# Kernel optimization log

Hardware: AMD Instinct MI355X
Metric: run time of the kernel (lower is better)

## Reference

```python
import jax, jax.numpy as jnp
import numpy as np

K = 1.0        # Lorentz manifold curvature parameter
EPS = 1e-7     # arccosh argument clamp (geoopt float32 eps)


def projx(x):
    # Project onto the hyperboloid: x0 = sqrt(K + ||x_1:||^2)
    rest = x[..., 1:]
    x0 = jnp.sqrt(K + jnp.sum(rest * rest, axis=-1, keepdims=True))
    return jnp.concatenate([x0, rest], axis=-1)


def setup_inputs() -> dict:
    key = jax.random.key(0)
    k1, k2 = jax.random.split(key)
    B, C, D = 16384, 2048, 512
    x = jax.random.normal(k1, (B, D), dtype=jnp.float32)
    # ManifoldParameter: random_normal with std = 1/sqrt(n_dim)
    points = jax.random.normal(k2, (C, D), dtype=jnp.float32) * (1.0 / np.sqrt(D))
    return {"x": x, "points": points}


def reference(x, points):
    xp = projx(x)        # (B, D) on hyperboloid
    pp = projx(points)   # (C, D) on hyperboloid
    # Minkowski inner <x,p>_L = -x0*p0 + sum_{i>0} x_i p_i = x.p - 2*x0*p0
    # Computed as a GEMM plus a rank-1 correction (avoids (B,C,D) intermediate).
    inner = xp @ pp.T - 2.0 * jnp.outer(xp[:, 0], pp[:, 0])  # (B, C)
    d = jnp.sqrt(K) * jnp.arccosh(jnp.maximum(-inner / K, 1.0 + EPS))
    return -d  # (B, C) negative Riemannian distances (class logits)
```

## Files before the change

kernel.cpp:

```cpp
#include <hip/hip_runtime.h>
#include <hip/hip_bf16.h>
#include <stdint.h>

#define B_ROWS 16384
#define C_ROWS 2048
#define D_FULL 512
#define KP     512

#define BM 128
#define BN 128
#define BK 64

typedef __attribute__((ext_vector_type(8))) short bf16x8;
typedef __attribute__((ext_vector_type(4))) float f32x4;

typedef __attribute__((address_space(1))) void glb_void;
typedef __attribute__((address_space(3))) void lds_void;

__device__ __forceinline__ void gld16(const void* g, void* l) {
    __builtin_amdgcn_global_load_lds((glb_void*)(uintptr_t)g,
                                     (lds_void*)(uintptr_t)l, 16, 0, 0);
}

__global__ __launch_bounds__(256) void prep_kernel(
    const float* __restrict__ x, const float* __restrict__ pts,
    unsigned short* __restrict__ Abf, unsigned short* __restrict__ Bbf,
    float* __restrict__ xn, float* __restrict__ pn)
{
    int row = blockIdx.x;
    const float* src;
    unsigned short* dst;
    float* nrm;
    if (row < B_ROWS) {
        src = x + (size_t)row * D_FULL;
        dst = Abf + (size_t)row * KP;
        nrm = xn + row;
    } else {
        int r = row - B_ROWS;
        src = pts + (size_t)r * D_FULL;
        dst = Bbf + (size_t)r * KP;
        nrm = pn + r;
    }
    int t = threadIdx.x;
    float v0 = src[t + 1];
    float v1 = (t < 255) ? src[t + 257] : 0.0f;
    __hip_bfloat16 b0 = __float2bfloat16(v0);
    __hip_bfloat16 b1 = __float2bfloat16(v1);
    dst[t]       = *(unsigned short*)&b0;
    dst[t + 256] = *(unsigned short*)&b1;
    float ss = v0 * v0 + v1 * v1;
    #pragma unroll
    for (int off = 32; off > 0; off >>= 1) ss += __shfl_down(ss, off);
    __shared__ float red[4];
    if ((t & 63) == 0) red[t >> 6] = ss;
    __syncthreads();
    if (t == 0) nrm[0] = sqrtf(1.0f + red[0] + red[1] + red[2] + red[3]);
}

__global__ __launch_bounds__(256) void gemm_kernel(
    const unsigned short* __restrict__ A,
    const unsigned short* __restrict__ Bm,
    const float* __restrict__ xn, const float* __restrict__ pn,
    float* __restrict__ out)
{
    __shared__ unsigned short As[BM * BK];
    __shared__ unsigned short Bs[BN * BK];

    const int tid  = threadIdx.x;
    const int wave = tid >> 6;
    const int lane = tid & 63;
    const int wm   = wave >> 1;
    const int wn   = wave & 1;
    const int lrow = lane & 15;
    const int quad = lane >> 4;

    const int bm0 = blockIdx.x * BM;
    const int bn0 = blockIdx.y * BN;

    const int srow = wave * 32 + (lane >> 3);
    const int scol = (lane & 7) * 8;

    const unsigned short* gA = A  + (size_t)(bm0 + srow) * KP + scol;
    const unsigned short* gB = Bm + (size_t)(bn0 + srow) * KP + scol;

    f32x4 acc[4][4] = {};

    for (int k0 = 0; k0 < KP; k0 += BK) {
        __syncthreads();
        #pragma unroll
        for (int i = 0; i < 4; ++i) {
            gld16(gA + (size_t)(i * 8) * KP + k0, &As[(wave * 32 + i * 8) * BK]);
            gld16(gB + (size_t)(i * 8) * KP + k0, &Bs[(wave * 32 + i * 8) * BK]);
        }
        __syncthreads();

        #pragma unroll
        for (int kk = 0; kk < BK; kk += 32) {
            bf16x8 af[4], bfr[4];
            #pragma unroll
            for (int mi = 0; mi < 4; ++mi)
                af[mi] = *(const bf16x8*)&As[(wm * 64 + mi * 16 + lrow) * BK + kk + quad * 8];
            #pragma unroll
            for (int ni = 0; ni < 4; ++ni)
                bfr[ni] = *(const bf16x8*)&Bs[(wn * 64 + ni * 16 + lrow) * BK + kk + quad * 8];
            #pragma unroll
            for (int mi = 0; mi < 4; ++mi)
                #pragma unroll
                for (int ni = 0; ni < 4; ++ni)
                    acc[mi][ni] = __builtin_amdgcn_mfma_f32_16x16x32_bf16(
                        af[mi], bfr[ni], acc[mi][ni], 0, 0, 0);
        }
    }

    float pv[4];
    #pragma unroll
    for (int ni = 0; ni < 4; ++ni)
        pv[ni] = pn[bn0 + wn * 64 + ni * 16 + lrow];

    #pragma unroll
    for (int mi = 0; mi < 4; ++mi) {
        #pragma unroll
        for (int r = 0; r < 4; ++r) {
            int row = bm0 + wm * 64 + mi * 16 + quad * 4 + r;
            float xv = xn[row];
            size_t base = (size_t)row * C_ROWS + bn0 + wn * 64 + lrow;
            #pragma unroll
            for (int ni = 0; ni < 4; ++ni) {
                float z = fmaf(xv, pv[ni], -acc[mi][ni][r]);
                z = fmaxf(z, 1.0f + 1e-7f);
                out[base + ni * 16] = -__logf(z + __fsqrt_rn(z * z - 1.0f));
            }
        }
    }
}

extern "C" void kernel_launch(void* const* d_in, const int* in_sizes, int n_in,
                              void* d_out, int out_size, void* d_ws, size_t ws_size,
                              hipStream_t stream) {
    const float* x   = (const float*)d_in[0];
    const float* pts = (const float*)d_in[1];
    float* out = (float*)d_out;

    char* ws = (char*)d_ws;
    unsigned short* Abf = (unsigned short*)ws;
    unsigned short* Bbf = (unsigned short*)(ws + (size_t)B_ROWS * KP * 2);
    float* xn = (float*)(ws + (size_t)(B_ROWS + C_ROWS) * KP * 2);
    float* pn = (float*)((char*)xn + (size_t)B_ROWS * 4);
    (void)in_sizes; (void)n_in; (void)out_size; (void)ws_size;

    prep_kernel<<<B_ROWS + C_ROWS, 256, 0, stream>>>(x, pts, Abf, Bbf, xn, pn);

    dim3 grid(B_ROWS / BM, C_ROWS / BN);
    gemm_kernel<<<grid, 256, 0, stream>>>(Abf, Bbf, xn, pn, out);
}
```

Baseline: 209.0 us.

## Load GEMM fragments directly from global memory with register prefetch

```diff
diff --git a/kernel.cpp b/kernel.cpp
--- a/kernel.cpp
+++ b/kernel.cpp
@@ -9,18 +9,9 @@
 
 #define BM 128
 #define BN 128
-#define BK 64
 
 typedef __attribute__((ext_vector_type(8))) short bf16x8;
 typedef __attribute__((ext_vector_type(4))) float f32x4;
-
-typedef __attribute__((address_space(1))) void glb_void;
-typedef __attribute__((address_space(3))) void lds_void;
-
-__device__ __forceinline__ void gld16(const void* g, void* l) {
-    __builtin_amdgcn_global_load_lds((glb_void*)(uintptr_t)g,
-                                     (lds_void*)(uintptr_t)l, 16, 0, 0);
-}
 
 __global__ __launch_bounds__(256) void prep_kernel(
     const float* __restrict__ x, const float* __restrict__ pts,
@@ -42,12 +33,14 @@
         nrm = pn + r;
     }
     int t = threadIdx.x;
-    float v0 = src[t + 1];
-    float v1 = (t < 255) ? src[t + 257] : 0.0f;
+    float v0 = src[2 * t + 1];
+    float v1 = (t < 255) ? src[2 * t + 2] : 0.0f;
     __hip_bfloat16 b0 = __float2bfloat16(v0);
     __hip_bfloat16 b1 = __float2bfloat16(v1);
-    dst[t]       = *(unsigned short*)&b0;
-    dst[t + 256] = *(unsigned short*)&b1;
+    union { unsigned short u[2]; unsigned int w; } pack;
+    pack.u[0] = *(unsigned short*)&b0;
+    pack.u[1] = *(unsigned short*)&b1;
+    *(unsigned int*)&dst[2 * t] = pack.w;
     float ss = v0 * v0 + v1 * v1;
     #pragma unroll
     for (int off = 32; off > 0; off >>= 1) ss += __shfl_down(ss, off);
@@ -63,9 +56,6 @@
     const float* __restrict__ xn, const float* __restrict__ pn,
     float* __restrict__ out)
 {
-    __shared__ unsigned short As[BM * BK];
-    __shared__ unsigned short Bs[BN * BK];
-
     const int tid  = threadIdx.x;
     const int wave = tid >> 6;
     const int lane = tid & 63;
@@ -74,43 +64,49 @@
     const int lrow = lane & 15;
     const int quad = lane >> 4;
 
-    const int bm0 = blockIdx.x * BM;
-    const int bn0 = blockIdx.y * BN;
+    const int bn0 = blockIdx.x * BN;
+    const int bm0 = blockIdx.y * BM;
 
-    const int srow = wave * 32 + (lane >> 3);
-    const int scol = (lane & 7) * 8;
-
-    const unsigned short* gA = A  + (size_t)(bm0 + srow) * KP + scol;
-    const unsigned short* gB = Bm + (size_t)(bn0 + srow) * KP + scol;
+    const unsigned short* aBase[4];
+    const unsigned short* bBase[4];
+    #pragma unroll
+    for (int i = 0; i < 4; ++i) {
+        aBase[i] = A  + (size_t)(bm0 + wm * 64 + i * 16 + lrow) * KP + quad * 8;
+        bBase[i] = Bm + (size_t)(bn0 + wn * 64 + i * 16 + lrow) * KP + quad * 8;
+    }
 
     f32x4 acc[4][4] = {};
 
-    for (int k0 = 0; k0 < KP; k0 += BK) {
-        __syncthreads();
+    bf16x8 a_cur[4], b_cur[4];
+    #pragma unroll
+    for (int i = 0; i < 4; ++i) {
+        a_cur[i] = *(const bf16x8*)(aBase[i]);
+        b_cur[i] = *(const bf16x8*)(bBase[i]);
+    }
+
+    #pragma unroll 2
+    for (int k = 32; k < KP; k += 32) {
+        bf16x8 a_nxt[4], b_nxt[4];
         #pragma unroll
         for (int i = 0; i < 4; ++i) {
-            gld16(gA + (size_t)(i * 8) * KP + k0, &As[(wave * 32 + i * 8) * BK]);
-            gld16(gB + (size_t)(i * 8) * KP + k0, &Bs[(wave * 32 + i * 8) * BK]);
+            a_nxt[i] = *(const bf16x8*)(aBase[i] + k);
+            b_nxt[i] = *(const bf16x8*)(bBase[i] + k);
         }
-        __syncthreads();
-
         #pragma unroll
-        for (int kk = 0; kk < BK; kk += 32) {
-            bf16x8 af[4], bfr[4];
-            #pragma unroll
-            for (int mi = 0; mi < 4; ++mi)
-                af[mi] = *(const bf16x8*)&As[(wm * 64 + mi * 16 + lrow) * BK + kk + quad * 8];
+        for (int mi = 0; mi < 4; ++mi)
             #pragma unroll
             for (int ni = 0; ni < 4; ++ni)
-                bfr[ni] = *(const bf16x8*)&Bs[(wn * 64 + ni * 16 + lrow) * BK + kk + quad * 8];
-            #pragma unroll
-            for (int mi = 0; mi < 4; ++mi)
-                #pragma unroll
-                for (int ni = 0; ni < 4; ++ni)
-                    acc[mi][ni] = __builtin_amdgcn_mfma_f32_16x16x32_bf16(
-                        af[mi], bfr[ni], acc[mi][ni], 0, 0, 0);
-        }
+                acc[mi][ni] = __builtin_amdgcn_mfma_f32_16x16x32_bf16(
+                    a_cur[mi], b_cur[ni], acc[mi][ni], 0, 0, 0);
+        #pragma unroll
+        for (int i = 0; i < 4; ++i) { a_cur[i] = a_nxt[i]; b_cur[i] = b_nxt[i]; }
     }
+    #pragma unroll
+    for (int mi = 0; mi < 4; ++mi)
+        #pragma unroll
+        for (int ni = 0; ni < 4; ++ni)
+            acc[mi][ni] = __builtin_amdgcn_mfma_f32_16x16x32_bf16(
+                a_cur[mi], b_cur[ni], acc[mi][ni], 0, 0, 0);
 
     float pv[4];
     #pragma unroll
@@ -150,6 +146,6 @@
 
     prep_kernel<<<B_ROWS + C_ROWS, 256, 0, stream>>>(x, pts, Abf, Bbf, xn, pn);
 
-    dim3 grid(B_ROWS / BM, C_ROWS / BN);
+    dim3 grid(C_ROWS / BN, B_ROWS / BM);
     gemm_kernel<<<grid, 256, 0, stream>>>(Abf, Bbf, xn, pn, out);
 }
```

Measured after the change: 277.1 us. +32.6%, slower.

## Double-buffer LDS tiles with swizzled layout and vectorize prep stores

Applied to the files above, without the earlier changes.

```diff
diff --git a/kernel.cpp b/kernel.cpp
--- a/kernel.cpp
+++ b/kernel.cpp
@@ -9,7 +9,7 @@
 
 #define BM 128
 #define BN 128
-#define BK 64
+#define BK 32
 
 typedef __attribute__((ext_vector_type(8))) short bf16x8;
 typedef __attribute__((ext_vector_type(4))) float f32x4;
@@ -42,12 +42,14 @@
         nrm = pn + r;
     }
     int t = threadIdx.x;
-    float v0 = src[t + 1];
-    float v1 = (t < 255) ? src[t + 257] : 0.0f;
+    float v0 = src[2 * t + 1];
+    float v1 = (t < 255) ? src[2 * t + 2] : 0.0f;
     __hip_bfloat16 b0 = __float2bfloat16(v0);
     __hip_bfloat16 b1 = __float2bfloat16(v1);
-    dst[t]       = *(unsigned short*)&b0;
-    dst[t + 256] = *(unsigned short*)&b1;
+    union { unsigned short u[2]; unsigned int w; } pack;
+    pack.u[0] = *(unsigned short*)&b0;
+    pack.u[1] = *(unsigned short*)&b1;
+    *(unsigned int*)&dst[2 * t] = pack.w;
     float ss = v0 * v0 + v1 * v1;
     #pragma unroll
     for (int off = 32; off > 0; off >>= 1) ss += __shfl_down(ss, off);
@@ -63,8 +65,8 @@
     const float* __restrict__ xn, const float* __restrict__ pn,
     float* __restrict__ out)
 {
-    __shared__ unsigned short As[BM * BK];
-    __shared__ unsigned short Bs[BN * BK];
+    __shared__ unsigned short As[2][BM * BK];
+    __shared__ unsigned short Bs[2][BN * BK];
 
     const int tid  = threadIdx.x;
     const int wave = tid >> 6;
@@ -77,39 +79,57 @@
     const int bm0 = blockIdx.x * BM;
     const int bn0 = blockIdx.y * BN;
 
-    const int srow = wave * 32 + (lane >> 3);
-    const int scol = (lane & 7) * 8;
+    const int srow  = lane >> 2;
+    const int schk  = (lane & 3) ^ (srow & 3) ^ ((lane >> 4) & 3);
+    const int scol  = schk << 3;
 
-    const unsigned short* gA = A  + (size_t)(bm0 + srow) * KP + scol;
-    const unsigned short* gB = Bm + (size_t)(bn0 + srow) * KP + scol;
+    const unsigned short* gA0 = A  + (size_t)(bm0 + wave * 32 + srow) * KP + scol;
+    const unsigned short* gA1 = gA0 + (size_t)16 * KP;
+    const unsigned short* gB0 = Bm + (size_t)(bn0 + wave * 32 + srow) * KP + scol;
+    const unsigned short* gB1 = gB0 + (size_t)16 * KP;
+
+    unsigned short* ldsA0 = &As[0][(wave * 32 + 0) * BK];
+    unsigned short* ldsA1 = &As[0][(wave * 32 + 16) * BK];
+    unsigned short* ldsB0 = &Bs[0][(wave * 32 + 0) * BK];
+    unsigned short* ldsB1 = &Bs[0][(wave * 32 + 16) * BK];
+    const int bufStride = BM * BK;
+
+    const int sw8 = ((quad ^ (lrow & 3) ^ (lrow >> 2)) & 3) << 3;
+
+    int aoff[4], boff[4];
+    #pragma unroll
+    for (int i = 0; i < 4; ++i) {
+        aoff[i] = (wm * 64 + i * 16 + lrow) * BK + sw8;
+        boff[i] = (wn * 64 + i * 16 + lrow) * BK + sw8;
+    }
 
     f32x4 acc[4][4] = {};
 
-    for (int k0 = 0; k0 < KP; k0 += BK) {
+    gld16(gA0, ldsA0); gld16(gA1, ldsA1);
+    gld16(gB0, ldsB0); gld16(gB1, ldsB1);
+
+    #pragma unroll 2
+    for (int it = 0; it < KP / BK; ++it) {
+        const int buf = it & 1;
         __syncthreads();
+        if (it + 1 < KP / BK) {
+            const int k1 = (it + 1) * BK;
+            const int d  = (buf ^ 1) * bufStride;
+            gld16(gA0 + k1, ldsA0 + d); gld16(gA1 + k1, ldsA1 + d);
+            gld16(gB0 + k1, ldsB0 + d); gld16(gB1 + k1, ldsB1 + d);
+        }
+        bf16x8 af[4], bfr[4];
         #pragma unroll
         for (int i = 0; i < 4; ++i) {
-            gld16(gA + (size_t)(i * 8) * KP + k0, &As[(wave * 32 + i * 8) * BK]);
-            gld16(gB + (size_t)(i * 8) * KP + k0, &Bs[(wave * 32 + i * 8) * BK]);
+            af[i]  = *(const bf16x8*)&As[buf][aoff[i]];
+            bfr[i] = *(const bf16x8*)&Bs[buf][boff[i]];
         }
-        __syncthreads();
-
         #pragma unroll
-        for (int kk = 0; kk < BK; kk += 32) {
-            bf16x8 af[4], bfr[4];
-            #pragma unroll
-            for (int mi = 0; mi < 4; ++mi)
-                af[mi] = *(const bf16x8*)&As[(wm * 64 + mi * 16 + lrow) * BK + kk + quad * 8];
+        for (int mi = 0; mi < 4; ++mi)
             #pragma unroll
             for (int ni = 0; ni < 4; ++ni)
-                bfr[ni] = *(const bf16x8*)&Bs[(wn * 64 + ni * 16 + lrow) * BK + kk + quad * 8];
-            #pragma unroll
-            for (int mi = 0; mi < 4; ++mi)
-                #pragma unroll
-                for (int ni = 0; ni < 4; ++ni)
-                    acc[mi][ni] = __builtin_amdgcn_mfma_f32_16x16x32_bf16(
-                        af[mi], bfr[ni], acc[mi][ni], 0, 0, 0);
-        }
+                acc[mi][ni] = __builtin_amdgcn_mfma_f32_16x16x32_bf16(
+                    af[mi], bfr[ni], acc[mi][ni], 0, 0, 0);
     }
 
     float pv[4];
```

Result: faster. 201.9 us (-3.4%).
